# Kernel tuning notes

Hardware: AMD Instinct MI355X
Metric: run time of the kernel (lower is better)

The kernel has to match this reference:

```python
import jax, jax.numpy as jnp
import numpy as np

B = 8192
N_COLS = 64
D = 1024
EPS = 1e-5


def _layernorm(x, g, b):
    m = jnp.mean(x, axis=-1, keepdims=True)
    v = jnp.mean(jnp.square(x - m), axis=-1, keepdims=True)
    return (x - m) * jax.lax.rsqrt(v + EPS) * g + b


def setup_inputs() -> dict:
    key = jax.random.key(0)
    ks = jax.random.split(key, 8)
    s = 0.02
    return {
        "x1_enc": jax.random.normal(ks[0], (1, N_COLS, D), jnp.float32),
        "x2_enc": jax.random.normal(ks[1], (B, D), jnp.float32),
        "We": jax.random.normal(ks[2], (4, 2 * D, D), jnp.float32) * s,
        "be": jnp.zeros((4, D), jnp.float32),
        "W1": jax.random.normal(ks[3], (2 * D, 4 * D), jnp.float32) * s,
        "b1": jnp.zeros((4 * D,), jnp.float32),
        "g1": jnp.ones((4 * D,), jnp.float32),
        "bt1": jnp.zeros((4 * D,), jnp.float32),
        "W2": jax.random.normal(ks[4], (4 * D, 2 * D), jnp.float32) * s,
        "b2": jnp.zeros((2 * D,), jnp.float32),
        "g2": jnp.ones((2 * D,), jnp.float32),
        "bt2": jnp.zeros((2 * D,), jnp.float32),
        "W3": jax.random.normal(ks[5], (2 * D, 1), jnp.float32) * s,
        "b3": jnp.zeros((1,), jnp.float32),
        "col_pairs": jax.random.randint(ks[6], (B, 2), 0, N_COLS, jnp.int64),
        "vis_type": jax.random.randint(ks[7], (B,), 0, 4, jnp.int64),
    }


def reference(x1_enc, x2_enc, We, be, W1, b1, g1, bt1, W2, b2, g2, bt2, W3, b3,
              col_pairs, vis_type):
    # x1 repeated B times is identical per row -> gather directly from x1_enc[0]
    x11 = x1_enc[0, col_pairs[:, 0]]          # [B, D]
    x12 = x1_enc[0, col_pairs[:, 1]]          # [B, D]
    x1c = jnp.concatenate([x11, x12], axis=1)  # [B, 2D]

    # 1-of-4 expert routing: compute all experts, select by vis_type
    all_y = jax.nn.relu(jnp.einsum('bd,edk->bek', x1c, We) + be)  # [B, 4, D]
    y1 = jnp.take_along_axis(all_y, vis_type[:, None, None], axis=1)[:, 0]  # [B, D]

    y = jnp.concatenate([y1, x2_enc], axis=1)  # [B, 2D]
    h = _layernorm(jax.nn.relu(y @ W1 + b1), g1, bt1)
    h = _layernorm(jax.nn.relu(h @ W2 + b2), g2, bt2)
    return jax.nn.sigmoid(h @ W3 + b3)  # [B, 1]
```

## Files before the change

kernel.cpp:

```cpp
#include <hip/hip_runtime.h>

typedef unsigned short u16;
typedef __bf16 bf16x8 __attribute__((ext_vector_type(8)));
typedef float f32x4v __attribute__((ext_vector_type(4)));
typedef u16 u16x8 __attribute__((ext_vector_type(8)));

__device__ __forceinline__ u16 f2bf(float f) {
  union { float f; unsigned u; } v; v.f = f;
  unsigned r = v.u + 0x7fffu + ((v.u >> 16) & 1u);
  return (u16)(r >> 16);
}
__device__ __forceinline__ float bf2f(u16 h) {
  union { unsigned u; float f; } v; v.u = ((unsigned)h) << 16;
  return v.f;
}

#define G2L16(g, l)                                                            \
  __builtin_amdgcn_global_load_lds((__attribute__((address_space(1))) void*)(g), \
                                   (__attribute__((address_space(3))) void*)(l), 16, 0, 0)

__global__ __launch_bounds__(256) void k_pre(const float* __restrict__ W1,
                                             u16* __restrict__ W1T,
                                             const float* __restrict__ W2,
                                             u16* __restrict__ W2gT,
                                             const float* __restrict__ g1,
                                             const float* __restrict__ bt1,
                                             float* __restrict__ w2ps,
                                             float* __restrict__ w2pc,
                                             const float* __restrict__ x1,
                                             const float* __restrict__ We,
                                             float* __restrict__ pq0,
                                             float* __restrict__ pq1) {
  __shared__ char smem[17536];
  const int t = threadIdx.x;
  int bid = blockIdx.x;
  if (bid < 4096) {
    float(*tile)[65] = (float(*)[65])smem;
    const float* in;
    u16* out;
    int R, C, bx, by, fold;
    if (bid < 2048) {
      in = W1; out = W1T; R = 2048; C = 4096; fold = 0;
      bx = bid & 63; by = bid >> 6;
    } else {
      bid -= 2048;
      in = W2; out = W2gT; R = 4096; C = 2048; fold = 1;
      bx = bid & 31; by = bid >> 5;
    }
    const int c0 = bx * 64, r0 = by * 64;
    const int tc = (t & 15) * 4, tr = t >> 4;
#pragma unroll
    for (int i = 0; i < 4; ++i) {
      int r = tr + i * 16;
      f32x4v v = *(const f32x4v*)(in + (size_t)(r0 + r) * C + c0 + tc);
      tile[r][tc] = v[0]; tile[r][tc + 1] = v[1];
      tile[r][tc + 2] = v[2]; tile[r][tc + 3] = v[3];
    }
    __syncthreads();
    const int oc = t >> 2;
    const int rb = (t & 3) * 16;
    float gv[16];
#pragma unroll
    for (int i = 0; i < 16; ++i) gv[i] = fold ? g1[r0 + rb + i] : 1.f;
    u16x8 o0, o1;
#pragma unroll
    for (int i = 0; i < 8; ++i) o0[i] = f2bf(tile[rb + i][oc] * gv[i]);
#pragma unroll
    for (int i = 0; i < 8; ++i) o1[i] = f2bf(tile[rb + 8 + i][oc] * gv[8 + i]);
    *(u16x8*)(out + (size_t)(c0 + oc) * R + r0 + rb) = o0;
    *(u16x8*)(out + (size_t)(c0 + oc) * R + r0 + rb + 8) = o1;
    if (fold) {
      float ps = 0.f, pc = 0.f;
#pragma unroll
      for (int i = 0; i < 16; ++i) {
        float w = tile[rb + i][oc];
        ps += gv[i] * w;
        pc += bt1[r0 + rb + i] * w;
      }
      ps += __shfl_down(ps, 2, 4); ps += __shfl_down(ps, 1, 4);
      pc += __shfl_down(pc, 2, 4); pc += __shfl_down(pc, 1, 4);
      if ((t & 3) == 0) {
        w2ps[(size_t)by * 2048 + c0 + oc] = ps;
        w2pc[(size_t)by * 2048 + c0 + oc] = pc;
      }
    }
  } else {
    const int idx = bid - 4096;
    const int n0 = (idx & 15) * 64;
    const int ep = (idx >> 4) & 7;
    const int e = ep >> 1, p = ep & 1;
    const int z = idx >> 7;
    const int ks = z * 512;
    float* pq = z ? pq1 : pq0;
    float(*As)[33] = (float(*)[33])smem;
    float(*Bs)[68] = (float(*)[68])(smem + 8448);
    const int tx = t & 15, ty = t >> 4;
    float acc[4][4] = {};
    const float* wbase = We + (size_t)e * 2048 * 1024 + (size_t)p * 1024 * 1024;
    for (int k0 = ks; k0 < ks + 512; k0 += 32) {
#pragma unroll
      for (int i = 0; i < 8; ++i) {
        int ix = t + i * 256;
        As[ix >> 5][ix & 31] = x1[(size_t)(ix >> 5) * 1024 + k0 + (ix & 31)];
      }
#pragma unroll
      for (int i = 0; i < 8; ++i) {
        int ix = t + i * 256;
        Bs[ix >> 6][ix & 63] = wbase[(size_t)(k0 + (ix >> 6)) * 1024 + n0 + (ix & 63)];
      }
      __syncthreads();
#pragma unroll
      for (int kk = 0; kk < 32; ++kk) {
        float av[4];
#pragma unroll
        for (int i = 0; i < 4; ++i) av[i] = As[ty * 4 + i][kk];
        f32x4v bv = *(const f32x4v*)&Bs[kk][tx * 4];
#pragma unroll
        for (int i = 0; i < 4; ++i)
#pragma unroll
          for (int j = 0; j < 4; ++j) acc[i][j] += av[i] * bv[j];
      }
      __syncthreads();
    }
#pragma unroll
    for (int i = 0; i < 4; ++i) {
      float* dst = pq + ((size_t)ep * 64 + ty * 4 + i) * 1024 + n0 + tx * 4;
#pragma unroll
      for (int j = 0; j < 4; ++j) dst[j] = acc[i][j];
    }
  }
}

__global__ __launch_bounds__(256) void k_build_y(const float* __restrict__ pq0,
                                                 const float* __restrict__ pq1,
                                                 const float* __restrict__ x2,
                                                 const float* __restrict__ be,
                                                 const int* __restrict__ cp,
                                                 const int* __restrict__ vis,
                                                 u16* __restrict__ Y) {
  const int t = threadIdx.x;
  for (int rr = 0; rr < 8; ++rr) {
    const int b = blockIdx.x * 8 + rr;
    const int e = vis[b];
    u16x8 o;
    if (t < 128) {
      const int c0 = cp[2 * b], c1 = cp[2 * b + 1];
      const size_t po = ((size_t)(e * 2) * 64 + c0) * 1024 + t * 8;
      const size_t qo = ((size_t)(e * 2 + 1) * 64 + c1) * 1024 + t * 8;
      const float* B = be + e * 1024 + t * 8;
#pragma unroll
      for (int i = 0; i < 8; ++i) {
        float v = pq0[po + i] + pq1[po + i] + pq0[qo + i] + pq1[qo + i] + B[i];
        o[i] = f2bf(v > 0.f ? v : 0.f);
      }
      *(u16x8*)(Y + (size_t)b * 2048 + t * 8) = o;
    } else {
      const float* X = x2 + (size_t)b * 1024 + (size_t)(t - 128) * 8;
#pragma unroll
      for (int i = 0; i < 8; ++i) o[i] = f2bf(X[i]);
      *(u16x8*)(Y + (size_t)b * 2048 + 1024 + (size_t)(t - 128) * 8) = o;
    }
  }
}

template <int MODE>
__global__ __launch_bounds__(256, 3) void k_gemm(const u16* __restrict__ A,
                                                 const u16* __restrict__ BT,
                                                 const float* __restrict__ bias,
                                                 const float2* __restrict__ stats,
                                                 const float* __restrict__ s1,
                                                 const float* __restrict__ c1b,
                                                 float2* __restrict__ sp_out,
                                                 u16* __restrict__ C, int M, int N, int K) {
  __shared__ u16 As[128 * 64];
  __shared__ u16 Bs[128 * 64];
  const int tid = threadIdx.x;
  const int lane = tid & 63;
  const int wave = tid >> 6;

  const int nx = gridDim.x, ny = gridDim.y;
  const int bid = blockIdx.y * nx + blockIdx.x;
  const int stripe = ny >> 3;
  const int xcd = bid & 7;
  const int loc = bid >> 3;
  const int panel = loc / (stripe * 4);
  const int rem = loc - panel * (stripe * 4);
  const int by = xcd * stripe + (rem >> 2);
  const int bx = panel * 4 + (rem & 3);
  const int tileN = bx * 128;
  const int tileM = by * 128;
  const int wm = wave & 1;
  const int wn = wave >> 1;

  f32x4v acc[4][4];
#pragma unroll
  for (int i = 0; i < 4; ++i)
#pragma unroll
    for (int j = 0; j < 4; ++j) acc[i][j] = (f32x4v){0.f, 0.f, 0.f, 0.f};

  const int srow = tid >> 3;
  const int lchunk = (tid & 7) ^ (srow & 7);
  const u16* aptr = A + (size_t)(tileM + srow) * K + lchunk * 8;
  const u16* bptr = BT + (size_t)(tileN + srow) * K + lchunk * 8;
  u16* asp = As + tid * 8;
  u16* bsp = Bs + tid * 8;

  const int s = lane & 7;
  const int kp0 = ((lane >> 4) ^ s) * 8;
  const int kp1 = kp0 ^ 32;
  const int am = wm * 64 + (lane & 15);
  const int bn = wn * 64 + (lane & 15);

  for (int k0 = 0; k0 < K; k0 += 64) {
    G2L16(aptr, asp);
    G2L16(aptr + (size_t)32 * K, asp + 2048);
    G2L16(aptr + (size_t)64 * K, asp + 4096);
    G2L16(aptr + (size_t)96 * K, asp + 6144);
    G2L16(bptr, bsp);
    G2L16(bptr + (size_t)32 * K, bsp + 2048);
    G2L16(bptr + (size_t)64 * K, bsp + 4096);
    G2L16(bptr + (size_t)96 * K, bsp + 6144);
    aptr += 64;
    bptr += 64;
    __syncthreads();

    bf16x8 af[4], bfr[4];
#pragma unroll
    for (int mi = 0; mi < 4; ++mi)
      af[mi] = *(const bf16x8*)(As + (am + mi * 16) * 64 + kp0);
#pragma unroll
    for (int ni = 0; ni < 4; ++ni)
      bfr[ni] = *(const bf16x8*)(Bs + (bn + ni * 16) * 64 + kp0);
#pragma unroll
    for (int mi = 0; mi < 4; ++mi)
#pragma unroll
      for (int ni = 0; ni < 4; ++ni)
        acc[mi][ni] = __builtin_amdgcn_mfma_f32_16x16x32_bf16(af[mi], bfr[ni], acc[mi][ni], 0, 0, 0);
#pragma unroll
    for (int mi = 0; mi < 4; ++mi)
      af[mi] = *(const bf16x8*)(As + (am + mi * 16) * 64 + kp1);
#pragma unroll
    for (int ni = 0; ni < 4; ++ni)
      bfr[ni] = *(const bf16x8*)(Bs + (bn + ni * 16) * 64 + kp1);
#pragma unroll
    for (int mi = 0; mi < 4; ++mi)
#pragma unroll
      for (int ni = 0; ni < 4; ++ni)
        acc[mi][ni] = __builtin_amdgcn_mfma_f32_16x16x32_bf16(af[mi], bfr[ni], acc[mi][ni], 0, 0, 0);
    __syncthreads();
  }

  const int crow = tileM + wm * 64 + (lane >> 4) * 4;
  const int ccol = tileN + wn * 64 + (lane & 15);
  float cv0[4], cv1[4];
#pragma unroll
  for (int ni = 0; ni < 4; ++ni) {
    const int c = ccol + ni * 16;
    if (MODE == 0) {
      cv0[ni] = bias[c];
    } else {
      cv0[ni] = s1[c];
      cv1[ni] = c1b[c];
    }
  }
  const int cb = bx * 2 + wn;
#pragma unroll
  for (int mi = 0; mi < 4; ++mi) {
#pragma unroll
    for (int r = 0; r < 4; ++r) {
      const int row = crow + mi * 16 + r;
      float m = 0.f, rs = 0.f;
      if (MODE == 1) {
        float2 st = stats[row];
        m = st.x; rs = st.y;
      }
      float s_ = 0.f, ss_ = 0.f;
#pragma unroll
      for (int ni = 0; ni < 4; ++ni) {
        float v;
        if (MODE == 0)
          v = acc[mi][ni][r] + cv0[ni];
        else
          v = rs * acc[mi][ni][r] - rs * m * cv0[ni] + cv1[ni];
        v = v > 0.f ? v : 0.f;
        if (MODE == 0) { s_ += v; ss_ += v * v; }
        C[(size_t)row * N + ccol + ni * 16] = f2bf(v);
      }
      if (MODE == 0) {
#pragma unroll
        for (int off = 8; off >= 1; off >>= 1) {
          s_ += __shfl_xor(s_, off, 16);
          ss_ += __shfl_xor(ss_, off, 16);
        }
        if ((lane & 15) == 0)
          sp_out[(size_t)cb * 8192 + row] = make_float2(s_, ss_);
      }
    }
  }
}

__global__ __launch_bounds__(256) void k_reduce(const float2* __restrict__ sp,
                                                float2* __restrict__ stats,
                                                const float* __restrict__ w2ps,
                                                const float* __restrict__ w2pc,
                                                const float* __restrict__ b2,
                                                float* __restrict__ s1,
                                                float* __restrict__ c1b) {
  const int bid = blockIdx.x;
  if (bid < 32) {
    const int row = bid * 256 + threadIdx.x;
    float s = 0.f, ss = 0.f;
    for (int cbk = 0; cbk < 64; ++cbk) {
      float2 p = sp[(size_t)cbk * 8192 + row];
      s += p.x; ss += p.y;
    }
    float m = s * (1.f / 4096.f);
    float var = ss * (1.f / 4096.f) - m * m;
    stats[row] = make_float2(m, rsqrtf(var + 1e-5f));
  } else {
    const int nn = (bid - 32) * 256 + threadIdx.x;
    float s = 0.f, c = 0.f;
    for (int kb = 0; kb < 64; ++kb) {
      s += w2ps[(size_t)kb * 2048 + nn];
      c += w2pc[(size_t)kb * 2048 + nn];
    }
    s1[nn] = s;
    c1b[nn] = c + b2[nn];
  }
}

__global__ __launch_bounds__(256) void k_ln_final(const u16* __restrict__ H2,
                                                  const float* __restrict__ g,
                                                  const float* __restrict__ bt,
                                                  const float* __restrict__ W3,
                                                  const float* __restrict__ b3,
                                                  float* __restrict__ out) {
  const int lane = threadIdx.x & 63;
  const int b = blockIdx.x * 4 + (threadIdx.x >> 6);
  const u16* row = H2 + (size_t)b * 2048;
  float vals[4][8];
  float s = 0.f, ss = 0.f;
#pragma unroll
  for (int c = 0; c < 4; ++c) {
    u16x8 v = *(const u16x8*)(row + c * 512 + lane * 8);
#pragma unroll
    for (int i = 0; i < 8; ++i) {
      float f = bf2f(v[i]);
      vals[c][i] = f;
      s += f;
      ss += f * f;
    }
  }
#pragma unroll
  for (int off = 32; off > 0; off >>= 1) {
    s += __shfl_down(s, off, 64);
    ss += __shfl_down(ss, off, 64);
  }
  s = __shfl(s, 0);
  ss = __shfl(ss, 0);
  const float m = s * (1.f / 2048.f);
  const float rs = rsqrtf(ss * (1.f / 2048.f) - m * m + 1e-5f);
  float dot = 0.f;
#pragma unroll
  for (int c = 0; c < 4; ++c)
#pragma unroll
    for (int i = 0; i < 8; ++i) {
      int col = c * 512 + lane * 8 + i;
      float h = (vals[c][i] - m) * rs * g[col] + bt[col];
      dot += h * W3[col];
    }
#pragma unroll
  for (int off = 32; off > 0; off >>= 1) dot += __shfl_down(dot, off, 64);
  if (lane == 0) out[b] = 1.f / (1.f + expf(-(dot + b3[0])));
}

extern "C" void kernel_launch(void* const* d_in, const int* in_sizes, int n_in,
                              void* d_out, int out_size, void* d_ws, size_t ws_size,
                              hipStream_t stream) {
  const float* x1 = (const float*)d_in[0];
  const float* x2 = (const float*)d_in[1];
  const float* We = (const float*)d_in[2];
  const float* be = (const float*)d_in[3];
  const float* W1 = (const float*)d_in[4];
  const float* b1 = (const float*)d_in[5];
  const float* g1 = (const float*)d_in[6];
  const float* bt1 = (const float*)d_in[7];
  const float* W2 = (const float*)d_in[8];
  const float* b2 = (const float*)d_in[9];
  const float* g2 = (const float*)d_in[10];
  const float* bt2 = (const float*)d_in[11];
  const float* W3 = (const float*)d_in[12];
  const float* b3 = (const float*)d_in[13];
  const int* cp = (const int*)d_in[14];
  const int* vis = (const int*)d_in[15];
  float* out = (float*)d_out;

  char* ws = (char*)d_ws;
  u16* W1T  = (u16*)(ws);
  u16* W2gT = (u16*)(ws + 16777216);
  u16* Y    = (u16*)(ws + 33554432);
  u16* H1   = (u16*)(ws + 67108864);
  float* PQ0 = (float*)(ws + 134217728);
  float* PQ1 = (float*)(ws + 136314880);
  float2* sp = (float2*)(ws + 134217728);
  float2* stats = (float2*)(ws + 138412032);
  float* s1   = (float*)(ws + 138477568);
  float* c1b  = (float*)(ws + 138485760);
  float* w2ps = (float*)(ws + 138493952);
  float* w2pc = (float*)(ws + 139018240);
  u16* H2 = Y;

  k_pre<<<4352, 256, 0, stream>>>(W1, W1T, W2, W2gT, g1, bt1, w2ps, w2pc,
                                  x1, We, PQ0, PQ1);
  k_build_y<<<1024, 256, 0, stream>>>(PQ0, PQ1, x2, be, cp, vis, Y);
  k_gemm<0><<<dim3(32, 64), 256, 0, stream>>>(
      Y, W1T, b1, nullptr, nullptr, nullptr, sp, H1, 8192, 4096, 2048);
  k_reduce<<<40, 256, 0, stream>>>(sp, stats, w2ps, w2pc, b2, s1, c1b);
  k_gemm<1><<<dim3(16, 64), 256, 0, stream>>>(
      H1, W2gT, nullptr, stats, s1, c1b, nullptr, H2, 8192, 2048, 4096);
  k_ln_final<<<2048, 256, 0, stream>>>(H2, g2, bt2, W3, b3, out);
}
```

Measured before the change: 497.6 us.

## Fold final LayerNorm and W3 projection into second GEMM epilogue

```diff
diff --git a/kernel.cpp b/kernel.cpp
--- a/kernel.cpp
+++ b/kernel.cpp
@@ -19,115 +19,115 @@
   __builtin_amdgcn_global_load_lds((__attribute__((address_space(1))) void*)(g), \
                                    (__attribute__((address_space(3))) void*)(l), 16, 0, 0)
 
-__global__ __launch_bounds__(256) void k_pre(const float* __restrict__ W1,
-                                             u16* __restrict__ W1T,
-                                             const float* __restrict__ W2,
-                                             u16* __restrict__ W2gT,
-                                             const float* __restrict__ g1,
-                                             const float* __restrict__ bt1,
-                                             float* __restrict__ w2ps,
-                                             float* __restrict__ w2pc,
-                                             const float* __restrict__ x1,
-                                             const float* __restrict__ We,
-                                             float* __restrict__ pq0,
-                                             float* __restrict__ pq1) {
-  __shared__ char smem[17536];
+__global__ __launch_bounds__(256) void k_transpose2(const float* __restrict__ W1,
+                                                    u16* __restrict__ W1T,
+                                                    const float* __restrict__ W2,
+                                                    u16* __restrict__ W2gT,
+                                                    const float* __restrict__ g1,
+                                                    const float* __restrict__ bt1,
+                                                    float* __restrict__ w2ps,
+                                                    float* __restrict__ w2pc) {
+  __shared__ float tile[64][65];
+  int bid = blockIdx.x;
+  const float* in;
+  u16* out;
+  int R, C, bx, by, fold;
+  if (bid < 2048) {
+    in = W1; out = W1T; R = 2048; C = 4096; fold = 0;
+    bx = bid & 63; by = bid >> 6;
+  } else {
+    bid -= 2048;
+    in = W2; out = W2gT; R = 4096; C = 2048; fold = 1;
+    bx = bid & 31; by = bid >> 5;
+  }
+  const int c0 = bx * 64, r0 = by * 64;
   const int t = threadIdx.x;
-  int bid = blockIdx.x;
-  if (bid < 4096) {
-    float(*tile)[65] = (float(*)[65])smem;
-    const float* in;
-    u16* out;
-    int R, C, bx, by, fold;
-    if (bid < 2048) {
-      in = W1; out = W1T; R = 2048; C = 4096; fold = 0;
-      bx = bid & 63; by = bid >> 6;
-    } else {
-      bid -= 2048;
-      in = W2; out = W2gT; R = 4096; C = 2048; fold = 1;
-      bx = bid & 31; by = bid >> 5;
-    }
-    const int c0 = bx * 64, r0 = by * 64;
-    const int tc = (t & 15) * 4, tr = t >> 4;
+  const int tc = (t & 15) * 4, tr = t >> 4;
+#pragma unroll
+  for (int i = 0; i < 4; ++i) {
+    int r = tr + i * 16;
+    f32x4v v = *(const f32x4v*)(in + (size_t)(r0 + r) * C + c0 + tc);
+    tile[r][tc] = v[0]; tile[r][tc + 1] = v[1];
+    tile[r][tc + 2] = v[2]; tile[r][tc + 3] = v[3];
+  }
+  __syncthreads();
+  const int oc = t >> 2;
+  const int rb = (t & 3) * 16;
+  float gv[16];
+#pragma unroll
+  for (int i = 0; i < 16; ++i) gv[i] = fold ? g1[r0 + rb + i] : 1.f;
+  u16x8 o0, o1;
+#pragma unroll
+  for (int i = 0; i < 8; ++i) o0[i] = f2bf(tile[rb + i][oc] * gv[i]);
+#pragma unroll
+  for (int i = 0; i < 8; ++i) o1[i] = f2bf(tile[rb + 8 + i][oc] * gv[8 + i]);
+  *(u16x8*)(out + (size_t)(c0 + oc) * R + r0 + rb) = o0;
+  *(u16x8*)(out + (size_t)(c0 + oc) * R + r0 + rb + 8) = o1;
+  if (fold) {
+    float ps = 0.f, pc = 0.f;
+#pragma unroll
+    for (int i = 0; i < 16; ++i) {
+      float w = tile[rb + i][oc];
+      ps += gv[i] * w;
+      pc += bt1[r0 + rb + i] * w;
+    }
+    ps += __shfl_down(ps, 2, 4); ps += __shfl_down(ps, 1, 4);
+    pc += __shfl_down(pc, 2, 4); pc += __shfl_down(pc, 1, 4);
+    if ((t & 3) == 0) {
+      w2ps[(size_t)by * 2048 + c0 + oc] = ps;
+      w2pc[(size_t)by * 2048 + c0 + oc] = pc;
+    }
+  }
+}
+
+__global__ __launch_bounds__(256) void k_pq(const float* __restrict__ x1,
+                                            const float* __restrict__ We,
+                                            float* __restrict__ pq0,
+                                            float* __restrict__ pq1) {
+  const int n0 = blockIdx.x * 64;
+  const int ep = blockIdx.y;
+  const int e = ep >> 1, p = ep & 1;
+  const int khalf = blockIdx.z & 1;
+  const int chalf = blockIdx.z >> 1;
+  const int ks = khalf * 512;
+  float* pq = khalf ? pq1 : pq0;
+  __shared__ float As[32][33];
+  __shared__ float Bs[32][68];
+  const int t = threadIdx.x;
+  const int tx = t & 15, ty = t >> 4;
+  float acc[2][4] = {};
+  const float* wbase = We + (size_t)e * 2048 * 1024 + (size_t)p * 1024 * 1024;
+  for (int k0 = ks; k0 < ks + 512; k0 += 32) {
 #pragma unroll
     for (int i = 0; i < 4; ++i) {
-      int r = tr + i * 16;
-      f32x4v v = *(const f32x4v*)(in + (size_t)(r0 + r) * C + c0 + tc);
-      tile[r][tc] = v[0]; tile[r][tc + 1] = v[1];
-      tile[r][tc + 2] = v[2]; tile[r][tc + 3] = v[3];
+      int ix = t + i * 256;
+      As[ix >> 5][ix & 31] =
+          x1[(size_t)(chalf * 32 + (ix >> 5)) * 1024 + k0 + (ix & 31)];
+    }
+#pragma unroll
+    for (int i = 0; i < 8; ++i) {
+      int ix = t + i * 256;
+      Bs[ix >> 6][ix & 63] = wbase[(size_t)(k0 + (ix >> 6)) * 1024 + n0 + (ix & 63)];
     }
     __syncthreads();
-    const int oc = t >> 2;
-    const int rb = (t & 3) * 16;
-    float gv[16];
-#pragma unroll
-    for (int i = 0; i < 16; ++i) gv[i] = fold ? g1[r0 + rb + i] : 1.f;
-    u16x8 o0, o1;
-#pragma unroll
-    for (int i = 0; i < 8; ++i) o0[i] = f2bf(tile[rb + i][oc] * gv[i]);
-#pragma unroll
-    for (int i = 0; i < 8; ++i) o1[i] = f2bf(tile[rb + 8 + i][oc] * gv[8 + i]);
-    *(u16x8*)(out + (size_t)(c0 + oc) * R + r0 + rb) = o0;
-    *(u16x8*)(out + (size_t)(c0 + oc) * R + r0 + rb + 8) = o1;
-    if (fold) {
-      float ps = 0.f, pc = 0.f;
-#pragma unroll
-      for (int i = 0; i < 16; ++i) {
-        float w = tile[rb + i][oc];
-        ps += gv[i] * w;
-        pc += bt1[r0 + rb + i] * w;
-      }
-      ps += __shfl_down(ps, 2, 4); ps += __shfl_down(ps, 1, 4);
-      pc += __shfl_down(pc, 2, 4); pc += __shfl_down(pc, 1, 4);
-      if ((t & 3) == 0) {
-        w2ps[(size_t)by * 2048 + c0 + oc] = ps;
-        w2pc[(size_t)by * 2048 + c0 + oc] = pc;
-      }
-    }
-  } else {
-    const int idx = bid - 4096;
-    const int n0 = (idx & 15) * 64;
-    const int ep = (idx >> 4) & 7;
-    const int e = ep >> 1, p = ep & 1;
-    const int z = idx >> 7;
-    const int ks = z * 512;
-    float* pq = z ? pq1 : pq0;
-    float(*As)[33] = (float(*)[33])smem;
-    float(*Bs)[68] = (float(*)[68])(smem + 8448);
-    const int tx = t & 15, ty = t >> 4;
-    float acc[4][4] = {};
-    const float* wbase = We + (size_t)e * 2048 * 1024 + (size_t)p * 1024 * 1024;
-    for (int k0 = ks; k0 < ks + 512; k0 += 32) {
-#pragma unroll
-      for (int i = 0; i < 8; ++i) {
-        int ix = t + i * 256;
-        As[ix >> 5][ix & 31] = x1[(size_t)(ix >> 5) * 1024 + k0 + (ix & 31)];
-      }
-#pragma unroll
-      for (int i = 0; i < 8; ++i) {
-        int ix = t + i * 256;
-        Bs[ix >> 6][ix & 63] = wbase[(size_t)(k0 + (ix >> 6)) * 1024 + n0 + (ix & 63)];
-      }
-      __syncthreads();
-#pragma unroll
-      for (int kk = 0; kk < 32; ++kk) {
-        float av[4];
-#pragma unroll
-        for (int i = 0; i < 4; ++i) av[i] = As[ty * 4 + i][kk];
-        f32x4v bv = *(const f32x4v*)&Bs[kk][tx * 4];
-#pragma unroll
-        for (int i = 0; i < 4; ++i)
-#pragma unroll
-          for (int j = 0; j < 4; ++j) acc[i][j] += av[i] * bv[j];
-      }
-      __syncthreads();
-    }
-#pragma unroll
-    for (int i = 0; i < 4; ++i) {
-      float* dst = pq + ((size_t)ep * 64 + ty * 4 + i) * 1024 + n0 + tx * 4;
-#pragma unroll
-      for (int j = 0; j < 4; ++j) dst[j] = acc[i][j];
-    }
+#pragma unroll
+    for (int kk = 0; kk < 32; ++kk) {
+      float av[2];
+#pragma unroll
+      for (int i = 0; i < 2; ++i) av[i] = As[ty * 2 + i][kk];
+      f32x4v bv = *(const f32x4v*)&Bs[kk][tx * 4];
+#pragma unroll
+      for (int i = 0; i < 2; ++i)
+#pragma unroll
+        for (int j = 0; j < 4; ++j) acc[i][j] += av[i] * bv[j];
+    }
+    __syncthreads();
+  }
+#pragma unroll
+  for (int i = 0; i < 2; ++i) {
+    float* dst = pq + ((size_t)ep * 64 + chalf * 32 + ty * 2 + i) * 1024 + n0 + tx * 4;
+#pragma unroll
+    for (int j = 0; j < 4; ++j) dst[j] = acc[i][j];
   }
 }
 
@@ -170,8 +170,11 @@
                                                  const float2* __restrict__ stats,
                                                  const float* __restrict__ s1,
                                                  const float* __restrict__ c1b,
+                                                 const float* __restrict__ gw3,
                                                  float2* __restrict__ sp_out,
-                                                 u16* __restrict__ C, int M, int N, int K) {
+                                                 float4* __restrict__ part,
+                                                 u16* __restrict__ C,
+                                                 int M, int N, int K) {
   __shared__ u16 As[128 * 64];
   __shared__ u16 Bs[128 * 64];
   const int tid = threadIdx.x;
@@ -252,7 +255,7 @@
 
   const int crow = tileM + wm * 64 + (lane >> 4) * 4;
   const int ccol = tileN + wn * 64 + (lane & 15);
-  float cv0[4], cv1[4];
+  float cv0[4], cv1[4], cg[4];
 #pragma unroll
   for (int ni = 0; ni < 4; ++ni) {
     const int c = ccol + ni * 16;
@@ -261,6 +264,7 @@
     } else {
       cv0[ni] = s1[c];
       cv1[ni] = c1b[c];
+      cg[ni] = gw3[c];
     }
   }
   const int cb = bx * 2 + wn;
@@ -269,31 +273,40 @@
 #pragma unroll
     for (int r = 0; r < 4; ++r) {
       const int row = crow + mi * 16 + r;
-      float m = 0.f, rs = 0.f;
-      if (MODE == 1) {
-        float2 st = stats[row];
-        m = st.x; rs = st.y;
-      }
-      float s_ = 0.f, ss_ = 0.f;
-#pragma unroll
-      for (int ni = 0; ni < 4; ++ni) {
-        float v;
-        if (MODE == 0)
-          v = acc[mi][ni][r] + cv0[ni];
-        else
-          v = rs * acc[mi][ni][r] - rs * m * cv0[ni] + cv1[ni];
-        v = v > 0.f ? v : 0.f;
-        if (MODE == 0) { s_ += v; ss_ += v * v; }
-        C[(size_t)row * N + ccol + ni * 16] = f2bf(v);
-      }
       if (MODE == 0) {
+        float s_ = 0.f, ss_ = 0.f;
+#pragma unroll
+        for (int ni = 0; ni < 4; ++ni) {
+          float v = acc[mi][ni][r] + cv0[ni];
+          v = v > 0.f ? v : 0.f;
+          s_ += v; ss_ += v * v;
+          C[(size_t)row * N + ccol + ni * 16] = f2bf(v);
+        }
 #pragma unroll
         for (int off = 8; off >= 1; off >>= 1) {
           s_ += __shfl_xor(s_, off, 16);
           ss_ += __shfl_xor(ss_, off, 16);
         }
         if ((lane & 15) == 0)
-          sp_out[(size_t)cb * 8192 + row] = make_float2(s_, ss_);
+          sp_out[(size_t)row * 64 + cb] = make_float2(s_, ss_);
+      } else {
+        float2 st = stats[row];
+        const float m = st.x, rs = st.y;
+        float s_ = 0.f, ss_ = 0.f, d_ = 0.f;
+#pragma unroll
+        for (int ni = 0; ni < 4; ++ni) {
+          float v = rs * acc[mi][ni][r] - rs * m * cv0[ni] + cv1[ni];
+          v = v > 0.f ? v : 0.f;
+          s_ += v; ss_ += v * v; d_ += v * cg[ni];
+        }
+#pragma unroll
+        for (int off = 8; off >= 1; off >>= 1) {
+          s_ += __shfl_xor(s_, off, 16);
+          ss_ += __shfl_xor(ss_, off, 16);
+          d_ += __shfl_xor(d_, off, 16);
+        }
+        if ((lane & 15) == 0)
+          part[(size_t)row * 32 + cb] = make_float4(s_, ss_, d_, 0.f);
       }
     }
   }
@@ -305,20 +318,39 @@
                                                 const float* __restrict__ w2pc,
                                                 const float* __restrict__ b2,
                                                 float* __restrict__ s1,
-                                                float* __restrict__ c1b) {
+                                                float* __restrict__ c1b,
+                                                const float* __restrict__ g2,
+                                                const float* __restrict__ bt2,
+                                                const float* __restrict__ W3,
+                                                float* __restrict__ gw3,
+                                                float* __restrict__ scal) {
+  __shared__ float red[8];
   const int bid = blockIdx.x;
+  const int t = threadIdx.x;
   if (bid < 32) {
-    const int row = bid * 256 + threadIdx.x;
-    float s = 0.f, ss = 0.f;
-    for (int cbk = 0; cbk < 64; ++cbk) {
-      float2 p = sp[(size_t)cbk * 8192 + row];
-      s += p.x; ss += p.y;
-    }
-    float m = s * (1.f / 4096.f);
-    float var = ss * (1.f / 4096.f) - m * m;
-    stats[row] = make_float2(m, rsqrtf(var + 1e-5f));
-  } else {
-    const int nn = (bid - 32) * 256 + threadIdx.x;
+    const int g = t >> 4, l = t & 15;
+#pragma unroll 1
+    for (int rr = 0; rr < 16; ++rr) {
+      const int row = bid * 256 + rr * 16 + g;
+      float s = 0.f, ss = 0.f;
+#pragma unroll
+      for (int i = 0; i < 4; ++i) {
+        float2 p = sp[(size_t)row * 64 + l * 4 + i];
+        s += p.x; ss += p.y;
+      }
+#pragma unroll
+      for (int off = 8; off >= 1; off >>= 1) {
+        s += __shfl_xor(s, off, 16);
+        ss += __shfl_xor(ss, off, 16);
+      }
+      if (l == 0) {
+        float m = s * (1.f / 4096.f);
+        float var = ss * (1.f / 4096.f) - m * m;
+        stats[row] = make_float2(m, rsqrtf(var + 1e-5f));
+      }
+    }
+  } else if (bid < 40) {
+    const int nn = (bid - 32) * 256 + t;
     float s = 0.f, c = 0.f;
     for (int kb = 0; kb < 64; ++kb) {
       s += w2ps[(size_t)kb * 2048 + nn];
@@ -326,52 +358,53 @@
     }
     s1[nn] = s;
     c1b[nn] = c + b2[nn];
-  }
-}
-
-__global__ __launch_bounds__(256) void k_ln_final(const u16* __restrict__ H2,
-                                                  const float* __restrict__ g,
-                                                  const float* __restrict__ bt,
-                                                  const float* __restrict__ W3,
-                                                  const float* __restrict__ b3,
-                                                  float* __restrict__ out) {
-  const int lane = threadIdx.x & 63;
-  const int b = blockIdx.x * 4 + (threadIdx.x >> 6);
-  const u16* row = H2 + (size_t)b * 2048;
-  float vals[4][8];
-  float s = 0.f, ss = 0.f;
-#pragma unroll
-  for (int c = 0; c < 4; ++c) {
-    u16x8 v = *(const u16x8*)(row + c * 512 + lane * 8);
-#pragma unroll
+  } else {
+    float sg = 0.f, cb = 0.f;
     for (int i = 0; i < 8; ++i) {
-      float f = bf2f(v[i]);
-      vals[c][i] = f;
-      s += f;
-      ss += f * f;
-    }
-  }
-#pragma unroll
-  for (int off = 32; off > 0; off >>= 1) {
-    s += __shfl_down(s, off, 64);
-    ss += __shfl_down(ss, off, 64);
-  }
-  s = __shfl(s, 0);
-  ss = __shfl(ss, 0);
-  const float m = s * (1.f / 2048.f);
-  const float rs = rsqrtf(ss * (1.f / 2048.f) - m * m + 1e-5f);
-  float dot = 0.f;
-#pragma unroll
-  for (int c = 0; c < 4; ++c)
-#pragma unroll
-    for (int i = 0; i < 8; ++i) {
-      int col = c * 512 + lane * 8 + i;
-      float h = (vals[c][i] - m) * rs * g[col] + bt[col];
-      dot += h * W3[col];
-    }
-#pragma unroll
-  for (int off = 32; off > 0; off >>= 1) dot += __shfl_down(dot, off, 64);
-  if (lane == 0) out[b] = 1.f / (1.f + expf(-(dot + b3[0])));
+      int c = i * 256 + t;
+      float w3 = W3[c];
+      float gv = g2[c] * w3;
+      gw3[c] = gv;
+      sg += gv;
+      cb += bt2[c] * w3;
+    }
+#pragma unroll
+    for (int off = 32; off > 0; off >>= 1) {
+      sg += __shfl_down(sg, off, 64);
+      cb += __shfl_down(cb, off, 64);
+    }
+    const int lane = t & 63, wv = t >> 6;
+    if (lane == 0) { red[wv] = sg; red[4 + wv] = cb; }
+    __syncthreads();
+    if (t == 0) {
+      scal[0] = red[0] + red[1] + red[2] + red[3];
+      scal[1] = red[4] + red[5] + red[6] + red[7];
+    }
+  }
+}
+
+__global__ __launch_bounds__(256) void k_final(const float4* __restrict__ part,
+                                               const float* __restrict__ scal,
+                                               const float* __restrict__ b3,
+                                               float* __restrict__ out) {
+  const int t = threadIdx.x;
+  const int g = t >> 4, l = t & 15;
+  const int row = blockIdx.x * 16 + g;
+  float4 a = part[(size_t)row * 32 + l * 2];
+  float4 b = part[(size_t)row * 32 + l * 2 + 1];
+  float S = a.x + b.x, SS = a.y + b.y, D = a.z + b.z;
+#pragma unroll
+  for (int off = 8; off >= 1; off >>= 1) {
+    S += __shfl_xor(S, off, 16);
+    SS += __shfl_xor(SS, off, 16);
+    D += __shfl_xor(D, off, 16);
+  }
+  if (l == 0) {
+    float m = S * (1.f / 2048.f);
+    float rs = rsqrtf(SS * (1.f / 2048.f) - m * m + 1e-5f);
+    float logit = rs * D - rs * m * scal[0] + scal[1] + b3[0];
+    out[row] = 1.f / (1.f + expf(-logit));
+  }
 }
 
 extern "C" void kernel_launch(void* const* d_in, const int* in_sizes, int n_in,
@@ -403,20 +436,25 @@
   float* PQ0 = (float*)(ws + 134217728);
   float* PQ1 = (float*)(ws + 136314880);
   float2* sp = (float2*)(ws + 134217728);
+  float4* part = (float4*)(ws + 134217728);
   float2* stats = (float2*)(ws + 138412032);
   float* s1   = (float*)(ws + 138477568);
   float* c1b  = (float*)(ws + 138485760);
   float* w2ps = (float*)(ws + 138493952);
   float* w2pc = (float*)(ws + 139018240);
-  u16* H2 = Y;
-
-  k_pre<<<4352, 256, 0, stream>>>(W1, W1T, W2, W2gT, g1, bt1, w2ps, w2pc,
-                                  x1, We, PQ0, PQ1);
+  float* gw3  = (float*)(ws + 139542528);
+  float* scal = (float*)(ws + 139550720);
+
+  k_transpose2<<<4096, 256, 0, stream>>>(W1, W1T, W2, W2gT, g1, bt1, w2ps, w2pc);
+  k_pq<<<dim3(16, 8, 4), 256, 0, stream>>>(x1, We, PQ0, PQ1);
   k_build_y<<<1024, 256, 0, stream>>>(PQ0, PQ1, x2, be, cp, vis, Y);
   k_gemm<0><<<dim3(32, 64), 256, 0, stream>>>(
-      Y, W1T, b1, nullptr, nullptr, nullptr, sp, H1, 8192, 4096, 2048);
-  k_reduce<<<40, 256, 0, stream>>>(sp, stats, w2ps, w2pc, b2, s1, c1b);
+      Y, W1T, b1, nullptr, nullptr, nullptr, nullptr, sp, nullptr, H1,
+      8192, 4096, 2048);
+  k_reduce<<<41, 256, 0, stream>>>(sp, stats, w2ps, w2pc, b2, s1, c1b,
+                                   g2, bt2, W3, gw3, scal);
   k_gemm<1><<<dim3(16, 64), 256, 0, stream>>>(
-      H1, W2gT, nullptr, stats, s1, c1b, nullptr, H2, 8192, 2048, 4096);
-  k_ln_final<<<2048, 256, 0, stream>>>(H2, g2, bt2, W3, b3, out);
-}
+      H1, W2gT, nullptr, stats, s1, c1b, gw3, nullptr, part, nullptr,
+      8192, 2048, 4096);
+  k_final<<<512, 256, 0, stream>>>(part, scal, b3, out);
+}
```

New measurement: 474.8 us. 4.6% less time.
